# Performance work log

Hardware: AMD Instinct MI355X
Metric: run time of the kernel (lower is better)

Reference implementation:

```python
import jax, jax.numpy as jnp
import numpy as np

N_NODES = 100_000
N_EDGES = 1_600_000
IN_F, OUT_F, EMB, ATT, MAX_R = 128, 64, 64, 32, 5
ALPHA = 0.2  # LeakyReLU negative slope


def setup_inputs() -> dict:
    key = jax.random.key(0)
    ks = jax.random.split(key, 8)
    inputs = jax.random.normal(ks[0], (N_NODES, IN_F), dtype=jnp.float32)
    edge = jax.random.randint(ks[1], (2, N_EDGES), 0, N_NODES, dtype=jnp.int32)
    review = jax.random.normal(ks[2], (N_EDGES, EMB), dtype=jnp.float32)
    rating = jax.random.uniform(ks[3], (N_EDGES, MAX_R), dtype=jnp.float32)
    u = lambda k, s: jax.random.uniform(k, s, dtype=jnp.float32, minval=-0.1, maxval=0.1)
    W = u(ks[4], (IN_F, OUT_F))
    a = u(ks[5], (2 * (OUT_F + ATT),))
    re_W = u(ks[6], (EMB, ATT))
    ra_W = u(ks[7], (MAX_R, ATT))
    return {"inputs": inputs, "edge": edge, "review": review, "rating": rating,
            "W": W, "a": a, "re_W": re_W, "ra_W": ra_W}


def reference(inputs, edge, review, rating, W, a, re_W, ra_W):
    N = inputs.shape[0]
    out_f = W.shape[1]
    att = re_W.shape[1]
    src, dst = edge[0], edge[1]  # row, col of COO adjacency

    h = inputs @ W            # [N, out_f]
    re_h = review @ re_W      # [E, att]
    ra_h = rating @ ra_W      # [E, att]

    # a @ concat(h[src], h[dst], re_h, ra_h)^T, computed without materializing the concat
    a_src = a[:out_f]
    a_dst = a[out_f:2 * out_f]
    a_re = a[2 * out_f:2 * out_f + att]
    a_ra = a[2 * out_f + att:]
    score = h[src] @ a_src + h[dst] @ a_dst + re_h @ a_re + ra_h @ a_ra  # [E]

    edge_e = jnp.exp(jax.nn.leaky_relu(score, negative_slope=ALPHA))  # [E]

    # sparse rowsum: A @ ones  -> segment_sum over row index
    e_rowsum = jax.ops.segment_sum(edge_e, src, num_segments=N) + 1e-10  # [N]
    # sparse weighted aggregation: A @ h  (dropout is identity in eval mode, p=0)
    h_prime = jax.ops.segment_sum(edge_e[:, None] * h[dst], src, num_segments=N)  # [N, out_f]
    h_prime = h_prime / e_rowsum[:, None] + h
    return jax.nn.elu(h_prime)  # concat=True
```

## Files before the change

kernel.cpp:

```cpp
#include <hip/hip_runtime.h>
#include <hip/hip_bf16.h>

#define N_NODES 100000
#define N_EDGES 1600000
#define IN_F 128
#define OUT_F 64
#define EMB 64
#define ATT 32
#define MAX_R 5
#define ALPHA 0.2f

__global__ __launch_bounds__(256) void k_gemm(const float* __restrict__ inp,
                                              const float* __restrict__ W,
                                              const float* __restrict__ a,
                                              float* __restrict__ h,
                                              float* __restrict__ s_src,
                                              float* __restrict__ s_dst) {
    __shared__ float Wl[IN_F * OUT_F];
    __shared__ float inl[4][IN_F];

    float4* Wl4 = (float4*)Wl;
    const float4* W4 = (const float4*)W;
#pragma unroll
    for (int i = 0; i < (IN_F * OUT_F / 4) / 256; ++i)
        Wl4[threadIdx.x + i * 256] = W4[threadIdx.x + i * 256];

    const int w = threadIdx.x >> 6, lane = threadIdx.x & 63;
    const int r = blockIdx.x * 4 + w;
    inl[w][lane]      = inp[(size_t)r * IN_F + lane];
    inl[w][64 + lane] = inp[(size_t)r * IN_F + 64 + lane];
    __syncthreads();

    float acc = 0.f;
#pragma unroll
    for (int k = 0; k < IN_F; ++k)
        acc = fmaf(inl[w][k], Wl[k * OUT_F + lane], acc);

    h[(size_t)r * OUT_F + lane] = acc;

    float ps = acc * a[lane];
    float pd = acc * a[64 + lane];
#pragma unroll
    for (int m = 32; m; m >>= 1) {
        ps += __shfl_xor(ps, m);
        pd += __shfl_xor(pd, m);
    }
    if (lane == 0) { s_src[r] = ps; s_dst[r] = pd; }
}

__global__ void k_vre(const float* __restrict__ re_W, const float* __restrict__ ra_W,
                      const float* __restrict__ a, float* __restrict__ v_re,
                      float* __restrict__ v_ra) {
    int t = threadIdx.x;
    if (t < EMB) {
        float s = 0.f;
        for (int j = 0; j < ATT; ++j) s = fmaf(re_W[t * ATT + j], a[2 * OUT_F + j], s);
        v_re[t] = s;
    } else if (t < EMB + MAX_R) {
        int m = t - EMB;
        float s = 0.f;
        for (int j = 0; j < ATT; ++j) s = fmaf(ra_W[m * ATT + j], a[2 * OUT_F + ATT + j], s);
        v_ra[m] = s;
    }
}

__global__ __launch_bounds__(256) void k_edge(const int* __restrict__ edge,
                                              const float* __restrict__ review,
                                              const float* __restrict__ rating,
                                              const float* __restrict__ s_src,
                                              const float* __restrict__ s_dst,
                                              const float* __restrict__ v_re,
                                              const float* __restrict__ v_ra,
                                              float* __restrict__ edge_e,
                                              int* __restrict__ counts) {
    const int g = threadIdx.x >> 4, sub = threadIdx.x & 15;
    const int e = blockIdx.x * 16 + g;

    float4 rv = ((const float4*)review)[(size_t)e * 16 + sub];
    float4 vr = ((const float4*)v_re)[sub];
    float p = rv.x * vr.x + rv.y * vr.y + rv.z * vr.z + rv.w * vr.w;
    if (sub < MAX_R) p = fmaf(rating[(size_t)e * MAX_R + sub], v_ra[sub], p);

    p += __shfl_xor(p, 1);
    p += __shfl_xor(p, 2);
    p += __shfl_xor(p, 4);
    p += __shfl_xor(p, 8);

    if (sub == 0) {
        int s = edge[e], d = edge[N_EDGES + e];
        float sc = p + s_src[s] + s_dst[d];
        sc = sc > 0.f ? sc : ALPHA * sc;
        float ee = __expf(sc);
        edge_e[e] = ee;
        atomicAdd(&counts[s], 1);
    }
}

__global__ __launch_bounds__(256) void k_scan1(const int* __restrict__ counts,
                                               int* __restrict__ offsets,
                                               int* __restrict__ bsums) {
    __shared__ int sh[256];
    int i = blockIdx.x * 256 + threadIdx.x;
    int v = (i < N_NODES) ? counts[i] : 0;
    sh[threadIdx.x] = v;
    __syncthreads();
    int incl = v;
#pragma unroll
    for (int d = 1; d < 256; d <<= 1) {
        int t = (threadIdx.x >= d) ? sh[threadIdx.x - d] : 0;
        __syncthreads();
        incl += t;
        sh[threadIdx.x] = incl;
        __syncthreads();
    }
    if (i < N_NODES) offsets[i] = incl - v;
    if (threadIdx.x == 255) bsums[blockIdx.x] = incl;
}

__global__ __launch_bounds__(512) void k_scan2(int* __restrict__ bsums, int nb) {
    __shared__ int sh[512];
    int t = threadIdx.x;
    int v = (t < nb) ? bsums[t] : 0;
    sh[t] = v;
    __syncthreads();
    int incl = v;
#pragma unroll
    for (int d = 1; d < 512; d <<= 1) {
        int x = (t >= d) ? sh[t - d] : 0;
        __syncthreads();
        incl += x;
        sh[t] = incl;
        __syncthreads();
    }
    if (t < nb) bsums[t] = incl - v;
}

__global__ __launch_bounds__(256) void k_scan3(int* __restrict__ offsets,
                                               int* __restrict__ cursors,
                                               const int* __restrict__ bsums) {
    int i = blockIdx.x * 256 + threadIdx.x;
    if (i < N_NODES) {
        int v = offsets[i] + bsums[blockIdx.x];
        offsets[i] = v;
        cursors[i] = v;
    }
    if (i == 0) offsets[N_NODES] = N_EDGES;
}

__global__ __launch_bounds__(256) void k_scatter(const int* __restrict__ edge,
                                                 const float* __restrict__ edge_e,
                                                 int* __restrict__ cursors,
                                                 int* __restrict__ sdst,
                                                 float* __restrict__ see) {
    int e = blockIdx.x * 256 + threadIdx.x;
    int s = edge[e];
    int pos = atomicAdd(&cursors[s], 1);
    sdst[pos] = edge[N_EDGES + e];
    see[pos] = edge_e[e];
}

__global__ __launch_bounds__(256) void k_aggregate(const int* __restrict__ offsets,
                                                   const int* __restrict__ sdst,
                                                   const float* __restrict__ see,
                                                   const float* __restrict__ h,
                                                   float* __restrict__ out) {
    const int lane = threadIdx.x & 63;
    const int w = __builtin_amdgcn_readfirstlane(threadIdx.x >> 6);
    const int n = blockIdx.x * 4 + w;
    int beg = offsets[n], end = offsets[n + 1];
    float acc = 0.f, rs = 1e-10f;
    for (int i = beg; i < end; ++i) {
        int d = sdst[i];
        float ee = see[i];
        rs += ee;
        acc = fmaf(ee, h[(size_t)d * OUT_F + lane], acc);
    }
    float hn = h[(size_t)n * OUT_F + lane];
    float v = acc / rs + hn;
    out[(size_t)n * OUT_F + lane] = v > 0.f ? v : expm1f(v);
}

extern "C" void kernel_launch(void* const* d_in, const int* in_sizes, int n_in,
                              void* d_out, int out_size, void* d_ws, size_t ws_size,
                              hipStream_t stream) {
    const float* inputs = (const float*)d_in[0];
    const int*   edge   = (const int*)d_in[1];
    const float* review = (const float*)d_in[2];
    const float* rating = (const float*)d_in[3];
    const float* W      = (const float*)d_in[4];
    const float* a      = (const float*)d_in[5];
    const float* re_W   = (const float*)d_in[6];
    const float* ra_W   = (const float*)d_in[7];
    float* out = (float*)d_out;

    char* ws = (char*)d_ws;
    size_t o = 0;
    auto alloc = [&](size_t bytes) -> void* {
        void* p = ws + o;
        o += (bytes + 255) & ~(size_t)255;
        return p;
    };
    float* h       = (float*)alloc((size_t)N_NODES * OUT_F * 4);
    float* s_src   = (float*)alloc((size_t)N_NODES * 4);
    float* s_dst   = (float*)alloc((size_t)N_NODES * 4);
    float* v_re    = (float*)alloc(EMB * 4);
    float* v_ra    = (float*)alloc(8 * 4);
    float* edge_e  = (float*)alloc((size_t)N_EDGES * 4);
    int*   counts  = (int*)alloc((size_t)(N_NODES + 1) * 4);
    int*   offsets = (int*)alloc((size_t)(N_NODES + 1) * 4);
    int*   cursors = (int*)alloc((size_t)(N_NODES + 1) * 4);
    int*   bsums   = (int*)alloc(512 * 4);
    int*   sdst    = (int*)alloc((size_t)N_EDGES * 4);
    float* see     = (float*)alloc((size_t)N_EDGES * 4);

    hipMemsetAsync(counts, 0, (size_t)N_NODES * 4, stream);

    k_gemm<<<N_NODES / 4, 256, 0, stream>>>(inputs, W, a, h, s_src, s_dst);
    k_vre<<<1, 128, 0, stream>>>(re_W, ra_W, a, v_re, v_ra);
    k_edge<<<N_EDGES / 16, 256, 0, stream>>>(edge, review, rating, s_src, s_dst,
                                             v_re, v_ra, edge_e, counts);
    int nb1 = (N_NODES + 255) / 256;
    k_scan1<<<nb1, 256, 0, stream>>>(counts, offsets, bsums);
    k_scan2<<<1, 512, 0, stream>>>(bsums, nb1);
    k_scan3<<<nb1, 256, 0, stream>>>(offsets, cursors, bsums);
    k_scatter<<<N_EDGES / 256, 256, 0, stream>>>(edge, edge_e, cursors, sdst, see);
    k_aggregate<<<N_NODES / 4, 256, 0, stream>>>(offsets, sdst, see, h, out);
}
```

Before: 953.2 us.

## Fuse edge scoring with CSR scatter, pack edge data, register-resident GEMM weights

Edge counting now runs as its own lightweight pass before the scan. The scoring kernel runs after the scan and writes (dst, weight) pairs straight into CSR order as packed int2, which removes the separate scatter pass and the edge_e round trip. The aggregation loop reads one packed entry per edge and is unrolled by two. The GEMM keeps a column of W in registers and loops over 10 rows per wave instead of staging W in LDS for every block. That raises register pressure and adds uncoalesced row reads, since each lane reads the same row address.

```diff
diff --git a/kernel.cpp b/kernel.cpp
--- a/kernel.cpp
+++ b/kernel.cpp
@@ -10,42 +10,44 @@
 #define MAX_R 5
 #define ALPHA 0.2f
 
+#define GEMM_RPW 10
+#define GEMM_BLOCKS (N_NODES / (4 * GEMM_RPW))
+
 __global__ __launch_bounds__(256) void k_gemm(const float* __restrict__ inp,
                                               const float* __restrict__ W,
                                               const float* __restrict__ a,
                                               float* __restrict__ h,
                                               float* __restrict__ s_src,
                                               float* __restrict__ s_dst) {
-    __shared__ float Wl[IN_F * OUT_F];
-    __shared__ float inl[4][IN_F];
-
-    float4* Wl4 = (float4*)Wl;
-    const float4* W4 = (const float4*)W;
-#pragma unroll
-    for (int i = 0; i < (IN_F * OUT_F / 4) / 256; ++i)
-        Wl4[threadIdx.x + i * 256] = W4[threadIdx.x + i * 256];
-
-    const int w = threadIdx.x >> 6, lane = threadIdx.x & 63;
-    const int r = blockIdx.x * 4 + w;
-    inl[w][lane]      = inp[(size_t)r * IN_F + lane];
-    inl[w][64 + lane] = inp[(size_t)r * IN_F + 64 + lane];
-    __syncthreads();
-
-    float acc = 0.f;
+    const int lane = threadIdx.x & 63;
+    const int wu = __builtin_amdgcn_readfirstlane(threadIdx.x >> 6);
+
+    float Wreg[IN_F];
 #pragma unroll
     for (int k = 0; k < IN_F; ++k)
-        acc = fmaf(inl[w][k], Wl[k * OUT_F + lane], acc);
-
-    h[(size_t)r * OUT_F + lane] = acc;
-
-    float ps = acc * a[lane];
-    float pd = acc * a[64 + lane];
-#pragma unroll
-    for (int m = 32; m; m >>= 1) {
-        ps += __shfl_xor(ps, m);
-        pd += __shfl_xor(pd, m);
-    }
-    if (lane == 0) { s_src[r] = ps; s_dst[r] = pd; }
+        Wreg[k] = W[k * OUT_F + lane];
+
+    const float asrc = a[lane], adst = a[OUT_F + lane];
+    const int r0 = (blockIdx.x * 4 + wu) * GEMM_RPW;
+
+    for (int j = 0; j < GEMM_RPW; ++j) {
+        const int r = r0 + j;
+        const float* __restrict__ row = inp + (size_t)r * IN_F;
+        float acc = 0.f;
+#pragma unroll
+        for (int k = 0; k < IN_F; ++k)
+            acc = fmaf(row[k], Wreg[k], acc);
+
+        h[(size_t)r * OUT_F + lane] = acc;
+
+        float ps = acc * asrc, pd = acc * adst;
+#pragma unroll
+        for (int m = 32; m; m >>= 1) {
+            ps += __shfl_xor(ps, m);
+            pd += __shfl_xor(pd, m);
+        }
+        if (lane == 0) { s_src[r] = ps; s_dst[r] = pd; }
+    }
 }
 
 __global__ void k_vre(const float* __restrict__ re_W, const float* __restrict__ ra_W,
@@ -64,36 +66,10 @@
     }
 }
 
-__global__ __launch_bounds__(256) void k_edge(const int* __restrict__ edge,
-                                              const float* __restrict__ review,
-                                              const float* __restrict__ rating,
-                                              const float* __restrict__ s_src,
-                                              const float* __restrict__ s_dst,
-                                              const float* __restrict__ v_re,
-                                              const float* __restrict__ v_ra,
-                                              float* __restrict__ edge_e,
-                                              int* __restrict__ counts) {
-    const int g = threadIdx.x >> 4, sub = threadIdx.x & 15;
-    const int e = blockIdx.x * 16 + g;
-
-    float4 rv = ((const float4*)review)[(size_t)e * 16 + sub];
-    float4 vr = ((const float4*)v_re)[sub];
-    float p = rv.x * vr.x + rv.y * vr.y + rv.z * vr.z + rv.w * vr.w;
-    if (sub < MAX_R) p = fmaf(rating[(size_t)e * MAX_R + sub], v_ra[sub], p);
-
-    p += __shfl_xor(p, 1);
-    p += __shfl_xor(p, 2);
-    p += __shfl_xor(p, 4);
-    p += __shfl_xor(p, 8);
-
-    if (sub == 0) {
-        int s = edge[e], d = edge[N_EDGES + e];
-        float sc = p + s_src[s] + s_dst[d];
-        sc = sc > 0.f ? sc : ALPHA * sc;
-        float ee = __expf(sc);
-        edge_e[e] = ee;
-        atomicAdd(&counts[s], 1);
-    }
+__global__ __launch_bounds__(256) void k_count(const int* __restrict__ edge,
+                                               int* __restrict__ counts) {
+    int e = blockIdx.x * 256 + threadIdx.x;
+    atomicAdd(&counts[edge[e]], 1);
 }
 
 __global__ __launch_bounds__(256) void k_scan1(const int* __restrict__ counts,
@@ -147,33 +123,61 @@
     if (i == 0) offsets[N_NODES] = N_EDGES;
 }
 
-__global__ __launch_bounds__(256) void k_scatter(const int* __restrict__ edge,
-                                                 const float* __restrict__ edge_e,
-                                                 int* __restrict__ cursors,
-                                                 int* __restrict__ sdst,
-                                                 float* __restrict__ see) {
-    int e = blockIdx.x * 256 + threadIdx.x;
-    int s = edge[e];
-    int pos = atomicAdd(&cursors[s], 1);
-    sdst[pos] = edge[N_EDGES + e];
-    see[pos] = edge_e[e];
+__global__ __launch_bounds__(256) void k_edge(const int* __restrict__ edge,
+                                              const float* __restrict__ review,
+                                              const float* __restrict__ rating,
+                                              const float* __restrict__ s_src,
+                                              const float* __restrict__ s_dst,
+                                              const float* __restrict__ v_re,
+                                              const float* __restrict__ v_ra,
+                                              int* __restrict__ cursors,
+                                              int2* __restrict__ packed) {
+    const int g = threadIdx.x >> 4, sub = threadIdx.x & 15;
+    const int e = blockIdx.x * 16 + g;
+
+    float4 rv = ((const float4*)review)[(size_t)e * 16 + sub];
+    float4 vr = ((const float4*)v_re)[sub];
+    float p = rv.x * vr.x + rv.y * vr.y + rv.z * vr.z + rv.w * vr.w;
+    if (sub < MAX_R) p = fmaf(rating[(size_t)e * MAX_R + sub], v_ra[sub], p);
+
+    p += __shfl_xor(p, 1);
+    p += __shfl_xor(p, 2);
+    p += __shfl_xor(p, 4);
+    p += __shfl_xor(p, 8);
+
+    if (sub == 0) {
+        int s = edge[e], d = edge[N_EDGES + e];
+        float sc = p + s_src[s] + s_dst[d];
+        sc = sc > 0.f ? sc : ALPHA * sc;
+        float ee = __expf(sc);
+        int pos = atomicAdd(&cursors[s], 1);
+        packed[pos] = make_int2(d, __float_as_int(ee));
+    }
 }
 
 __global__ __launch_bounds__(256) void k_aggregate(const int* __restrict__ offsets,
-                                                   const int* __restrict__ sdst,
-                                                   const float* __restrict__ see,
+                                                   const int2* __restrict__ packed,
                                                    const float* __restrict__ h,
                                                    float* __restrict__ out) {
     const int lane = threadIdx.x & 63;
-    const int w = __builtin_amdgcn_readfirstlane(threadIdx.x >> 6);
-    const int n = blockIdx.x * 4 + w;
+    const int wu = __builtin_amdgcn_readfirstlane(threadIdx.x >> 6);
+    const int n = blockIdx.x * 4 + wu;
     int beg = offsets[n], end = offsets[n + 1];
     float acc = 0.f, rs = 1e-10f;
-    for (int i = beg; i < end; ++i) {
-        int d = sdst[i];
-        float ee = see[i];
-        rs += ee;
-        acc = fmaf(ee, h[(size_t)d * OUT_F + lane], acc);
+    int i = beg;
+    for (; i + 2 <= end; i += 2) {
+        int2 p0 = packed[i], p1 = packed[i + 1];
+        float e0 = __int_as_float(p0.y), e1 = __int_as_float(p1.y);
+        float h0 = h[(size_t)p0.x * OUT_F + lane];
+        float h1 = h[(size_t)p1.x * OUT_F + lane];
+        rs += e0 + e1;
+        acc = fmaf(e0, h0, fmaf(e1, h1, acc));
+    }
+    if (i < end) {
+        int2 p0 = packed[i];
+        float e0 = __int_as_float(p0.y);
+        rs += e0;
+        acc = fmaf(e0, h[(size_t)p0.x * OUT_F + lane], acc);
     }
     float hn = h[(size_t)n * OUT_F + lane];
     float v = acc / rs + hn;
@@ -205,24 +209,22 @@
     float* s_dst   = (float*)alloc((size_t)N_NODES * 4);
     float* v_re    = (float*)alloc(EMB * 4);
     float* v_ra    = (float*)alloc(8 * 4);
-    float* edge_e  = (float*)alloc((size_t)N_EDGES * 4);
     int*   counts  = (int*)alloc((size_t)(N_NODES + 1) * 4);
     int*   offsets = (int*)alloc((size_t)(N_NODES + 1) * 4);
     int*   cursors = (int*)alloc((size_t)(N_NODES + 1) * 4);
     int*   bsums   = (int*)alloc(512 * 4);
-    int*   sdst    = (int*)alloc((size_t)N_EDGES * 4);
-    float* see     = (float*)alloc((size_t)N_EDGES * 4);
+    int2*  packed  = (int2*)alloc((size_t)N_EDGES * 8);
 
     hipMemsetAsync(counts, 0, (size_t)N_NODES * 4, stream);
 
-    k_gemm<<<N_NODES / 4, 256, 0, stream>>>(inputs, W, a, h, s_src, s_dst);
+    k_gemm<<<GEMM_BLOCKS, 256, 0, stream>>>(inputs, W, a, h, s_src, s_dst);
     k_vre<<<1, 128, 0, stream>>>(re_W, ra_W, a, v_re, v_ra);
-    k_edge<<<N_EDGES / 16, 256, 0, stream>>>(edge, review, rating, s_src, s_dst,
-                                             v_re, v_ra, edge_e, counts);
+    k_count<<<N_EDGES / 256, 256, 0, stream>>>(edge, counts);
     int nb1 = (N_NODES + 255) / 256;
     k_scan1<<<nb1, 256, 0, stream>>>(counts, offsets, bsums);
     k_scan2<<<1, 512, 0, stream>>>(bsums, nb1);
     k_scan3<<<nb1, 256, 0, stream>>>(offsets, cursors, bsums);
-    k_scatter<<<N_EDGES / 256, 256, 0, stream>>>(edge, edge_e, cursors, sdst, see);
-    k_aggregate<<<N_NODES / 4, 256, 0, stream>>>(offsets, sdst, see, h, out);
-}
+    k_edge<<<N_EDGES / 16, 256, 0, stream>>>(edge, review, rating, s_src, s_dst,
+                                             v_re, v_ra, cursors, packed);
+    k_aggregate<<<N_NODES / 4, 256, 0, stream>>>(offsets, packed, h, out);
+}
```

New measurement: 892.1 us. -6.4%, faster.
